# Optimization experiments

Hardware: AMD Instinct MI355X
Metric: run time of the kernel (lower is better)

## Reference

```python
import jax, jax.numpy as jnp
import numpy as np

N = 50000      # num nodes
E = 1600000    # num edges
F_IN = 512     # dataset.num_features
DIM = 512      # args.dim
C = 40         # dataset.num_classes


def setup_inputs() -> dict:
    key = jax.random.key(0)
    ks = jax.random.split(key, 5)
    x = jax.random.normal(ks[0], (N, F_IN), dtype=jnp.float32)
    edge_row = jax.random.randint(ks[1], (E,), 0, N, dtype=jnp.int64) if jax.config.jax_enable_x64 else jax.random.randint(ks[1], (E,), 0, N).astype(jnp.int32)
    edge_col = jax.random.randint(ks[2], (E,), 0, N).astype(edge_row.dtype)
    W1 = jax.random.normal(ks[3], (F_IN, DIM), dtype=jnp.float32) / np.float32(np.sqrt(F_IN))
    b1 = jnp.zeros((DIM,), jnp.float32)
    W2 = jax.random.normal(ks[4], (DIM * 5, C), dtype=jnp.float32) / np.float32(np.sqrt(DIM * 5))
    b2 = jnprz = jnp.zeros((C,), jnp.float32)
    return {"x": x, "edge_row": edge_row, "edge_col": edge_col,
            "W1": W1, "b1": b1, "W2": W2, "b2": b2}


def _gcn_norm(row, col, num_nodes):
    # PyG gcn_norm: add self-loops (weight 1), then D^-1/2 A D^-1/2
    loop = jnp.arange(num_nodes, dtype=row.dtype)
    row = jnp.concatenate([row, loop])
    col = jnp.concatenate([col, loop])
    ew = jnp.ones(row.shape[0], jnp.float32)
    deg = jax.ops.segment_sum(ew, col, num_segments=num_nodes)
    dinv = jnp.where(deg > 0, 1.0 / jnp.sqrt(deg), 0.0)
    val = dinv[row] * ew * dinv[col]
    return row, col, val


def _spmm(row, col, val, x):
    # out[i] = sum_{e: row[e]==i} val[e] * x[col[e]]
    return jax.ops.segment_sum(val[:, None] * x[col], row, num_segments=x.shape[0])


def reference(x, edge_row, edge_col, W1, b1, W2, b2):
    row, col, val = _gcn_norm(edge_row, edge_col, x.shape[0])
    t = jax.nn.relu(x @ W1 + b1)                      # [N, DIM]
    t1 = jnp.concatenate([t, _spmm(row, col, val, t)], axis=1)   # [N, 2*DIM]
    t2 = _spmm(row, col, val, t1)                     # [N, 2*DIM]
    h = jnp.concatenate([t, t1, t2], axis=1)          # [N, 5*DIM]
    # dropout treated as identity (deterministic eval reference)
    logits = h @ W2 + b2                              # [N, C]
    return jax.nn.log_softmax(logits, axis=1)
```

## Files before the change

kernel.cpp:

```cpp
#include <hip/hip_runtime.h>
#include <stdint.h>

#define NN 50000
#define NE 1600000
#define FI 512
#define DD 512
#define NC 40
#define SCAN_NB 49
#define CB 256
#define EPB (NE / CB)
#define HWRD 12500

typedef __attribute__((ext_vector_type(8))) short short8;
typedef __attribute__((ext_vector_type(4))) float float4v;
typedef __attribute__((ext_vector_type(2))) float f32x2;

static __device__ __forceinline__ unsigned short f2b(float f) {
    union { float f; unsigned int i; } v; v.f = f;
    unsigned int r = v.i + 0x7fffu + ((v.i >> 16) & 1u);
    return (unsigned short)(r >> 16);
}
static __device__ __forceinline__ float blo(unsigned int u) {
    union { unsigned int i; float f; } v; v.i = u << 16; return v.f;
}
static __device__ __forceinline__ float bhi(unsigned int u) {
    union { unsigned int i; float f; } v; v.i = u & 0xffff0000u; return v.f;
}
static __device__ __forceinline__ void async_copy16(void* lds, const void* g) {
    __builtin_amdgcn_global_load_lds((const __attribute__((address_space(1))) void*)g,
                                     (__attribute__((address_space(3))) void*)lds, 16, 0, 0);
}

__global__ __launch_bounds__(256) void mega1_kernel(
    const int* __restrict__ er, const int* __restrict__ ec,
    const float* __restrict__ x, const float* __restrict__ W1, const float* __restrict__ W2,
    unsigned char* __restrict__ rank, unsigned* __restrict__ hist_row, unsigned* __restrict__ hist_col,
    unsigned short* __restrict__ xb, unsigned short* __restrict__ w1t, unsigned short* __restrict__ wcpt) {
    __shared__ unsigned hb[HWRD];
    int bid = blockIdx.x, tid = threadIdx.x;
    if (bid < 2 * CB) {
        for (int w = tid; w < HWRD; w += 256) hb[w] = 0;
        __syncthreads();
        int b = bid & (CB - 1);
        int e0 = b * EPB;
        if (bid < CB) {
            for (int e = e0 + tid; e < e0 + EPB; e += 256) {
                int r = er[e];
                unsigned sh = (r & 3) * 8;
                unsigned old = atomicAdd(&hb[r >> 2], 1u << sh);
                rank[e] = (unsigned char)((old >> sh) & 0xFFu);
            }
        } else {
            for (int e = e0 + tid; e < e0 + EPB; e += 256) {
                int c = ec[e];
                atomicAdd(&hb[c >> 2], 1u << ((c & 3) * 8));
            }
        }
        __syncthreads();
        unsigned* dst = (bid < CB ? hist_row : hist_col) + (size_t)b * HWRD;
        for (int w = tid; w < HWRD; w += 256) dst[w] = hb[w];
        return;
    }
    bid -= 2 * CB;
    if (bid < 12500) {
        int t = bid * 256 + tid;
        const float* xf = x + (size_t)t * 8;
        float4 v0 = *(const float4*)(xf);
        float4 v1 = *(const float4*)(xf + 4);
        uint4 u;
        u.x = ((unsigned)f2b(v0.y) << 16) | f2b(v0.x);
        u.y = ((unsigned)f2b(v0.w) << 16) | f2b(v0.z);
        u.z = ((unsigned)f2b(v1.y) << 16) | f2b(v1.x);
        u.w = ((unsigned)f2b(v1.w) << 16) | f2b(v1.z);
        *(uint4*)(xb + (size_t)t * 8) = u;
        return;
    }
    bid -= 12500;
    if (bid < 1024) {
        int t = bid * 256 + tid;
        int n = t & 511, k = t >> 9;
        w1t[n * 512 + k] = f2b(W1[(size_t)k * 512 + n]);
        return;
    }
    bid -= 1024;
    {
        int t = bid * 256 + tid;
        int n = t >> 9, k = t & 511;
        float v = 0.f;
        if (n < 40)       v = W2[(size_t)k * NC + n] + W2[(size_t)(k + 512) * NC + n];
        else if (n < 80)  v = W2[(size_t)(k + 1024) * NC + (n - 40)] + W2[(size_t)(k + 1536) * NC + (n - 40)];
        else if (n < 120) v = W2[(size_t)(k + 2048) * NC + (n - 80)];
        wcpt[n * 512 + k] = f2b(v);
    }
}

__global__ __launch_bounds__(256) void prep_kernel(
    const unsigned* __restrict__ hist_row, const unsigned* __restrict__ hist_col,
    unsigned* __restrict__ base_words, int* __restrict__ cntI, int* __restrict__ degI) {
    int t = blockIdx.x * 256 + threadIdx.x;
    if (t < HWRD) {
        unsigned acc = 0;
        for (int b = 0; b < CB; ++b) {
            unsigned h = hist_row[(size_t)b * HWRD + t];
            base_words[(size_t)b * HWRD + t] = acc;
            acc += h;
        }
        int4 o; o.x = acc & 0xFF; o.y = (acc >> 8) & 0xFF; o.z = (acc >> 16) & 0xFF; o.w = (acc >> 24) & 0xFF;
        ((int4*)cntI)[t] = o;
    } else if (t < 2 * HWRD) {
        int w = t - HWRD;
        unsigned acc = 0;
        for (int b = 0; b < CB; ++b) acc += hist_col[(size_t)b * HWRD + w];
        int4 o; o.x = acc & 0xFF; o.y = (acc >> 8) & 0xFF; o.z = (acc >> 16) & 0xFF; o.w = (acc >> 24) & 0xFF;
        ((int4*)degI)[w] = o;
    }
}

__global__ __launch_bounds__(1024) void scan1_kernel(const int* __restrict__ cnt,
                                                     int* __restrict__ excl, int* __restrict__ bsum) {
    __shared__ int buf[1024];
    int tid = threadIdx.x, gid = blockIdx.x * 1024 + tid;
    int v = (gid < NN) ? cnt[gid] : 0;
    buf[tid] = v;
    __syncthreads();
    int acc = v;
    for (int off = 1; off < 1024; off <<= 1) {
        int t = (tid >= off) ? buf[tid - off] : 0;
        __syncthreads();
        acc += t;
        buf[tid] = acc;
        __syncthreads();
    }
    if (gid < NN) excl[gid] = acc - v;
    if (tid == 1023) bsum[blockIdx.x] = acc;
}

__global__ void scan2_kernel(const int* __restrict__ bsum, int* __restrict__ boff) {
    int tid = threadIdx.x;
    int orig = (tid < SCAN_NB) ? bsum[tid] : 0;
    int v = orig;
    #pragma unroll
    for (int off = 1; off < 64; off <<= 1) {
        int t = __shfl_up(v, off, 64);
        if (tid >= off) v += t;
    }
    if (tid < SCAN_NB) boff[tid] = v - orig;
}

__global__ void scan3_kernel(int* __restrict__ rowptr, const int* __restrict__ boff,
                             const int* __restrict__ deg, float* __restrict__ dinv) {
    int gid = blockIdx.x * 256 + threadIdx.x;
    if (gid < NN) {
        rowptr[gid] += boff[gid >> 10];
        dinv[gid] = rsqrtf((float)(deg[gid] + 1));
    }
    if (gid == 0) rowptr[NN] = NE;
}

__global__ __launch_bounds__(256) void mega2_kernel(
    const int* __restrict__ er, const int* __restrict__ ec, const int* __restrict__ rowptr,
    const unsigned char* __restrict__ rank, const unsigned char* __restrict__ base8,
    int* __restrict__ colss,
    const unsigned short* __restrict__ xb, const unsigned short* __restrict__ w1t,
    const float* __restrict__ b1, unsigned short* __restrict__ tbuf) {
    __shared__ __align__(16) unsigned short As[128 * 32];
    __shared__ __align__(16) unsigned short Bs[128 * 32];
    int bid = blockIdx.x;
    if (bid < CB) {
        int tid = threadIdx.x;
        const unsigned char* bb = base8 + (size_t)bid * 50000;
        int e0 = bid * EPB;
        int e = e0 + tid;
        #pragma unroll 4
        for (int it = 0; it < EPB / 256; ++it, e += 256) {
            int r = er[e], c = ec[e];
            colss[rowptr[r] + (int)bb[r] + (int)rank[e]] = c;
        }
        if (e < e0 + EPB) {
            int r = er[e], c = ec[e];
            colss[rowptr[r] + (int)bb[r] + (int)rank[e]] = c;
        }
        return;
    }
    bid -= CB;
    const int m0 = (bid >> 2) * 128, n0 = (bid & 3) * 128;
    const int tid = threadIdx.x;
    const int wave = tid >> 6, lane = tid & 63;
    const int q = lane >> 4, c = lane & 15;
    const int wm = wave & 1, wn = wave >> 1;

    float4v acc[4][4];
    for (int i = 0; i < 4; ++i)
        for (int j = 0; j < 4; ++j)
            acc[i][j] = (float4v){0.f, 0.f, 0.f, 0.f};

    for (int k0 = 0; k0 < FI; k0 += 32) {
        __syncthreads();
        #pragma unroll
        for (int h = 0; h < 2; ++h) {
            int chunk = h * 256 + wave * 64 + lane;
            int r = chunk >> 2, kc = chunk & 3;
            int gm = m0 + r; gm = gm < NN ? gm : NN - 1;
            async_copy16((char*)As + (size_t)(h * 256 + wave * 64) * 16,
                         xb + (size_t)gm * FI + k0 + kc * 8);
            async_copy16((char*)Bs + (size_t)(h * 256 + wave * 64) * 16,
                         w1t + (size_t)(n0 + r) * FI + k0 + kc * 8);
        }
        __syncthreads();
        short8 a[4], b[4];
        #pragma unroll
        for (int mi = 0; mi < 4; ++mi)
            a[mi] = *(const short8*)(As + ((wm * 64 + mi * 16 + c) * 32 + q * 8));
        #pragma unroll
        for (int ni = 0; ni < 4; ++ni)
            b[ni] = *(const short8*)(Bs + ((wn * 64 + ni * 16 + c) * 32 + q * 8));
        #pragma unroll
        for (int mi = 0; mi < 4; ++mi)
            #pragma unroll
            for (int ni = 0; ni < 4; ++ni)
                acc[mi][ni] = __builtin_amdgcn_mfma_f32_16x16x32_bf16(a[mi], b[ni], acc[mi][ni], 0, 0, 0);
    }
    #pragma unroll
    for (int ni = 0; ni < 4; ++ni) {
        int col = n0 + wn * 64 + ni * 16 + c;
        float bias = b1[col];
        #pragma unroll
        for (int mi = 0; mi < 4; ++mi) {
            int rbase = m0 + wm * 64 + mi * 16 + q * 4;
            #pragma unroll
            for (int r = 0; r < 4; ++r) {
                int row = rbase + r;
                if (row < NN) {
                    float v = acc[mi][ni][r] + bias;
                    v = v > 0.f ? v : 0.f;
                    tbuf[(size_t)row * FI + col] = f2b(v);
                }
            }
        }
    }
}

__global__ __launch_bounds__(256) void proj_kernel(
    const unsigned short* __restrict__ tb, const unsigned short* __restrict__ wcpt,
    const float* __restrict__ dinv, float* __restrict__ d0f,
    unsigned short* __restrict__ zs12p) {
    int wave = threadIdx.x >> 6, lane = threadIdx.x & 63;
    int q = lane >> 4, c = lane & 15;
    int row0 = blockIdx.x * 64 + wave * 16;
    int ra = row0 + c; ra = ra < NN ? ra : NN - 1;
    const unsigned short* ap = tb + (size_t)ra * FI + q * 8;

    float4v A[8];
    #pragma unroll
    for (int g = 0; g < 8; ++g) A[g] = (float4v){0.f, 0.f, 0.f, 0.f};
    #pragma unroll 2
    for (int k0 = 0; k0 < 512; k0 += 32) {
        short8 a = *(const short8*)(ap + k0);
        #pragma unroll
        for (int g = 0; g < 8; ++g) {
            short8 b = *(const short8*)(wcpt + (size_t)(g * 16 + c) * 512 + q * 8 + k0);
            A[g] = __builtin_amdgcn_mfma_f32_16x16x32_bf16(a, b, A[g], 0, 0, 0);
        }
    }
    #pragma unroll
    for (int r = 0; r < 4; ++r) {
        int rowg = row0 + q * 4 + r;
        if (rowg < NN) {
            float dv = dinv[rowg];
            #pragma unroll
            for (int g = 0; g < 8; ++g) {
                int j = g * 16 + c;
                float pv = A[g][r];
                if (j < 40)      d0f[(size_t)rowg * 40 + j] = pv;
                else if (j < 80) zs12p[(size_t)rowg * 128 + (j - 40)] = f2b(dv * pv);
                else             zs12p[(size_t)rowg * 128 + (j - 16)] = f2b(dv * pv);
            }
        }
    }
    for (int idx = lane; idx < 16 * 40; idx += 64) {
        int rr = row0 + idx / 40, pc = idx % 40;
        if (rr < NN) zs12p[(size_t)rr * 128 + (pc < 24 ? 40 + pc : 88 + pc)] = 0;
    }
}

__global__ __launch_bounds__(256) void spmma_kernel(
    const unsigned* __restrict__ zs,
    const int* __restrict__ rowptr, const int* __restrict__ cols,
    const float* __restrict__ dinv,
    float* __restrict__ u1b,
    unsigned* __restrict__ wpb) {
    int i = blockIdx.x * 4 + (threadIdx.x >> 6);
    if (i >= NN) return;
    int lane = threadIdx.x & 63;
    int h = lane >> 5, l = lane & 31;
    const float di = dinv[i];
    const unsigned* base = zs + l * 2;

    float a0 = 0.f, a1 = 0.f, a2 = 0.f, a3 = 0.f;
    float b0 = 0.f, b1 = 0.f, b2 = 0.f, b3 = 0.f;
    if (h == 0) {
        uint2 u = *(const uint2*)(zs + (size_t)i * 64 + l * 2);
        a0 = blo(u.x); a1 = bhi(u.x); a2 = blo(u.y); a3 = bhi(u.y);
    }
    int k = rowptr[i], e = rowptr[i + 1];
    for (; k + 8 <= e; k += 8) {
        int c0 = cols[k + h], c1 = cols[k + 2 + h], c2 = cols[k + 4 + h], c3 = cols[k + 6 + h];
        uint2 g0 = *(const uint2*)(base + (size_t)c0 * 64);
        uint2 g1 = *(const uint2*)(base + (size_t)c1 * 64);
        uint2 g2 = *(const uint2*)(base + (size_t)c2 * 64);
        uint2 g3 = *(const uint2*)(base + (size_t)c3 * 64);
        a0 += blo(g0.x); a1 += bhi(g0.x); a2 += blo(g0.y); a3 += bhi(g0.y);
        b0 += blo(g1.x); b1 += bhi(g1.x); b2 += blo(g1.y); b3 += bhi(g1.y);
        a0 += blo(g2.x); a1 += bhi(g2.x); a2 += blo(g2.y); a3 += bhi(g2.y);
        b0 += blo(g3.x); b1 += bhi(g3.x); b2 += blo(g3.y); b3 += bhi(g3.y);
    }
    for (; k + 2 <= e; k += 2) {
        int cc = cols[k + h];
        uint2 g = *(const uint2*)(base + (size_t)cc * 64);
        a0 += blo(g.x); a1 += bhi(g.x); a2 += blo(g.y); a3 += bhi(g.y);
    }
    if (k < e && h == 0) {
        int cc = cols[k];
        uint2 g = *(const uint2*)(base + (size_t)cc * 64);
        a0 += blo(g.x); a1 += bhi(g.x); a2 += blo(g.y); a3 += bhi(g.y);
    }
    a0 += b0; a1 += b1; a2 += b2; a3 += b3;
    a0 += __shfl_xor(a0, 32, 64); a1 += __shfl_xor(a1, 32, 64);
    a2 += __shfl_xor(a2, 32, 64); a3 += __shfl_xor(a3, 32, 64);
    if (h == 0) {
        if (l < 10) {
            float4 o; o.x = di * a0; o.y = di * a1; o.z = di * a2; o.w = di * a3;
            *(float4*)(u1b + (size_t)i * 40 + l * 4) = o;
        } else if (l >= 16) {
            float s = di * di;
            uint2 o;
            o.x = ((unsigned)f2b(s * a1) << 16) | f2b(s * a0);
            o.y = ((unsigned)f2b(s * a3) << 16) | f2b(s * a2);
            *(uint2*)(wpb + (size_t)i * 32 + (size_t)(l - 16) * 2) = o;
        }
    }
}

__global__ __launch_bounds__(256) void spmmb_kernel(
    const unsigned* __restrict__ wpb,
    const int* __restrict__ rowptr, const int* __restrict__ cols,
    const float* __restrict__ dinv, const float* __restrict__ d0f,
    const float* __restrict__ u1b, const float* __restrict__ b2p,
    float* __restrict__ out) {
    int i = blockIdx.x * 4 + (threadIdx.x >> 6);
    if (i >= NN) return;
    int lane = threadIdx.x & 63;
    int q = lane >> 4, l = lane & 15;
    const float di = dinv[i];
    const unsigned* base = wpb + l * 2;

    float a0 = 0.f, a1 = 0.f, a2 = 0.f, a3 = 0.f;
    float b0 = 0.f, b1 = 0.f, b2 = 0.f, b3 = 0.f;
    if (q == 0) {
        uint2 u = *(const uint2*)(wpb + (size_t)i * 32 + l * 2);
        a0 = blo(u.x); a1 = bhi(u.x); a2 = blo(u.y); a3 = bhi(u.y);
    }
    int k = rowptr[i], e = rowptr[i + 1];
    for (; k + 8 <= e; k += 8) {
        int c0 = cols[k + q], c1 = cols[k + 4 + q];
        uint2 g0 = *(const uint2*)(base + (size_t)c0 * 32);
        uint2 g1 = *(const uint2*)(base + (size_t)c1 * 32);
        a0 += blo(g0.x); a1 += bhi(g0.x); a2 += blo(g0.y); a3 += bhi(g0.y);
        b0 += blo(g1.x); b1 += bhi(g1.x); b2 += blo(g1.y); b3 += bhi(g1.y);
    }
    for (; k + 4 <= e; k += 4) {
        int cc = cols[k + q];
        uint2 g = *(const uint2*)(base + (size_t)cc * 32);
        a0 += blo(g.x); a1 += bhi(g.x); a2 += blo(g.y); a3 += bhi(g.y);
    }
    if (k + q < e) {
        int cc = cols[k + q];
        uint2 g = *(const uint2*)(base + (size_t)cc * 32);
        a0 += blo(g.x); a1 += bhi(g.x); a2 += blo(g.y); a3 += bhi(g.y);
    }
    a0 += b0; a1 += b1; a2 += b2; a3 += b3;
    a0 += __shfl_xor(a0, 16, 64); a1 += __shfl_xor(a1, 16, 64);
    a2 += __shfl_xor(a2, 16, 64); a3 += __shfl_xor(a3, 16, 64);
    a0 += __shfl_xor(a0, 32, 64); a1 += __shfl_xor(a1, 32, 64);
    a2 += __shfl_xor(a2, 32, 64); a3 += __shfl_xor(a3, 32, 64);

    float v0 = -1e30f, v1 = -1e30f, v2 = -1e30f, v3 = -1e30f;
    bool act = (q == 0) && (l < 10);
    if (act) {
        float4 dd = *(const float4*)(d0f + (size_t)i * 40 + l * 4);
        float4 uu = *(const float4*)(u1b + (size_t)i * 40 + l * 4);
        float4 bb = *(const float4*)(b2p + l * 4);
        v0 = dd.x + uu.x + di * a0 + bb.x;
        v1 = dd.y + uu.y + di * a1 + bb.y;
        v2 = dd.z + uu.z + di * a2 + bb.z;
        v3 = dd.w + uu.w + di * a3 + bb.w;
    }
    float mx = fmaxf(fmaxf(v0, v1), fmaxf(v2, v3));
    #pragma unroll
    for (int d = 1; d < 64; d <<= 1) mx = fmaxf(mx, __shfl_xor(mx, d, 64));
    float s = act ? (__expf(v0 - mx) + __expf(v1 - mx) + __expf(v2 - mx) + __expf(v3 - mx)) : 0.f;
    #pragma unroll
    for (int d = 1; d < 64; d <<= 1) s += __shfl_xor(s, d, 64);
    float lse = mx + __logf(s);
    if (act) {
        float4 o; o.x = v0 - lse; o.y = v1 - lse; o.z = v2 - lse; o.w = v3 - lse;
        *(float4*)(out + (size_t)i * 40 + l * 4) = o;
    }
}

extern "C" void kernel_launch(void* const* d_in, const int* in_sizes, int n_in,
                              void* d_out, int out_size, void* d_ws, size_t ws_size,
                              hipStream_t stream) {
    const float* x  = (const float*)d_in[0];
    const int*   er = (const int*)d_in[1];
    const int*   ec = (const int*)d_in[2];
    const float* W1 = (const float*)d_in[3];
    const float* b1 = (const float*)d_in[4];
    const float* W2 = (const float*)d_in[5];
    const float* b2 = (const float*)d_in[6];
    float* out = (float*)d_out;

    char* p = (char*)d_ws;
    auto alloc = [&](size_t bytes) { char* r = p; p += (bytes + 255) & ~((size_t)255); return r; };
    int*      cntI   = (int*)      alloc((size_t)NN * 4);
    int*      degI   = (int*)      alloc((size_t)NN * 4);
    int*      rowptr = (int*)      alloc((size_t)(NN + 1) * 4);
    float*    dinv   = (float*)    alloc((size_t)NN * 4);
    int*      bsum   = (int*)      alloc((size_t)SCAN_NB * 4);
    int*      boff   = (int*)      alloc((size_t)SCAN_NB * 4);
    unsigned char* rank = (unsigned char*)alloc((size_t)NE);
    int*      colss  = (int*)      alloc((size_t)NE * 4);
    unsigned* hist_row = (unsigned*)alloc((size_t)CB * HWRD * 4);
    unsigned* hist_col = (unsigned*)alloc((size_t)CB * HWRD * 4);
    unsigned* base_w   = (unsigned*)alloc((size_t)CB * HWRD * 4);
    unsigned short* w1t  = (unsigned short*)alloc((size_t)512 * 512 * 2);
    unsigned short* wcpt = (unsigned short*)alloc((size_t)128 * 512 * 2);
    unsigned short* xb   = (unsigned short*)alloc((size_t)NN * FI * 2);
    unsigned short* tbuf = (unsigned short*)alloc((size_t)NN * FI * 2);
    unsigned short* zs12p = (unsigned short*)alloc((size_t)NN * 128 * 2);
    float*    d0f  = (float*)alloc((size_t)NN * 40 * 4);
    float*    u1b  = (float*)alloc((size_t)NN * 40 * 4);
    unsigned* wpb  = (unsigned*)alloc((size_t)NN * 32 * 4);

    mega1_kernel<<<2 * CB + 12500 + 1024 + 256, 256, 0, stream>>>(
        er, ec, x, W1, W2, rank, hist_row, hist_col, xb, w1t, wcpt);
    prep_kernel<<<(2 * HWRD + 255) / 256, 256, 0, stream>>>(hist_row, hist_col, base_w, cntI, degI);
    scan1_kernel<<<SCAN_NB, 1024, 0, stream>>>(cntI, rowptr, bsum);
    scan2_kernel<<<1, 64, 0, stream>>>(bsum, boff);
    scan3_kernel<<<(NN + 255) / 256, 256, 0, stream>>>(rowptr, boff, degI, dinv);
    mega2_kernel<<<CB + ((NN + 127) / 128) * 4, 256, 0, stream>>>(
        er, ec, rowptr, rank, (const unsigned char*)base_w, colss, xb, w1t, b1, tbuf);
    proj_kernel<<<(NN + 63) / 64, 256, 0, stream>>>(tbuf, wcpt, dinv, d0f, zs12p);
    spmma_kernel<<<(NN + 3) / 4, 256, 0, stream>>>((const unsigned*)zs12p, rowptr, colss, dinv, u1b, wpb);
    spmmb_kernel<<<(NN + 3) / 4, 256, 0, stream>>>(wpb, rowptr, colss, dinv, d0f, u1b, b2, out);
}
```

Before: 476.5 us.

## Compact sparse gather buffers and remap GEMM tiles to 128x64 with XCD-aware ordering

Shrinks the padded bf16 intermediate rows from 128 to 80 columns and the second-hop buffer from 32 to 20 words, so each SpMM gather moves fewer bytes per edge. The second SpMM now gives each lane 2 classes and splits edges across two half-waves instead of four quarter-waves. The first GEMM switches to 128x64 tiles and a block-index remap that groups M tiles by XCD, aiming for better L2 reuse of rows of x. The 80-column row stride is not a multiple of 128 bytes, so gathers may become less aligned, and the smaller tiles mean more blocks with less reuse per block.

```diff
diff --git a/kernel.cpp b/kernel.cpp
--- a/kernel.cpp
+++ b/kernel.cpp
@@ -10,6 +10,8 @@
 #define CB 256
 #define EPB (NE / CB)
 #define HWRD 12500
+#define MT 391
+#define GEMMB 3136
 
 typedef __attribute__((ext_vector_type(8))) short short8;
 typedef __attribute__((ext_vector_type(4))) float float4v;
@@ -164,7 +166,7 @@
     const unsigned short* __restrict__ xb, const unsigned short* __restrict__ w1t,
     const float* __restrict__ b1, unsigned short* __restrict__ tbuf) {
     __shared__ __align__(16) unsigned short As[128 * 32];
-    __shared__ __align__(16) unsigned short Bs[128 * 32];
+    __shared__ __align__(16) unsigned short Bs[64 * 32];
     int bid = blockIdx.x;
     if (bid < CB) {
         int tid = threadIdx.x;
@@ -182,16 +184,21 @@
         }
         return;
     }
-    bid -= CB;
-    const int m0 = (bid >> 2) * 128, n0 = (bid & 3) * 128;
+    int gb = bid - CB;
+    int xcd = gb & 7, slot = gb >> 3;
+    int m = xcd + 8 * (slot >> 3), n = slot & 7;
+    if (m >= MT) return;
+    const int m0 = m * 128, n0 = n * 64;
     const int tid = threadIdx.x;
     const int wave = tid >> 6, lane = tid & 63;
     const int q = lane >> 4, c = lane & 15;
     const int wm = wave & 1, wn = wave >> 1;
 
-    float4v acc[4][4];
+    float4v acc[4][2];
+    #pragma unroll
     for (int i = 0; i < 4; ++i)
-        for (int j = 0; j < 4; ++j)
+        #pragma unroll
+        for (int j = 0; j < 2; ++j)
             acc[i][j] = (float4v){0.f, 0.f, 0.f, 0.f};
 
     for (int k0 = 0; k0 < FI; k0 += 32) {
@@ -201,28 +208,32 @@
             int chunk = h * 256 + wave * 64 + lane;
             int r = chunk >> 2, kc = chunk & 3;
             int gm = m0 + r; gm = gm < NN ? gm : NN - 1;
-            async_copy16((char*)As + (size_t)(h * 256 + wave * 64) * 16,
+            async_copy16((char*)As + (size_t)chunk * 16,
                          xb + (size_t)gm * FI + k0 + kc * 8);
-            async_copy16((char*)Bs + (size_t)(h * 256 + wave * 64) * 16,
-                         w1t + (size_t)(n0 + r) * FI + k0 + kc * 8);
-        }
-        __syncthreads();
-        short8 a[4], b[4];
+        }
+        {
+            int chunk = wave * 64 + lane;
+            int rb = chunk >> 2, kb = chunk & 3;
+            async_copy16((char*)Bs + (size_t)chunk * 16,
+                         w1t + (size_t)(n0 + rb) * FI + k0 + kb * 8);
+        }
+        __syncthreads();
+        short8 a[4], b[2];
         #pragma unroll
         for (int mi = 0; mi < 4; ++mi)
             a[mi] = *(const short8*)(As + ((wm * 64 + mi * 16 + c) * 32 + q * 8));
         #pragma unroll
-        for (int ni = 0; ni < 4; ++ni)
-            b[ni] = *(const short8*)(Bs + ((wn * 64 + ni * 16 + c) * 32 + q * 8));
+        for (int ni = 0; ni < 2; ++ni)
+            b[ni] = *(const short8*)(Bs + ((wn * 32 + ni * 16 + c) * 32 + q * 8));
         #pragma unroll
         for (int mi = 0; mi < 4; ++mi)
             #pragma unroll
-            for (int ni = 0; ni < 4; ++ni)
+            for (int ni = 0; ni < 2; ++ni)
                 acc[mi][ni] = __builtin_amdgcn_mfma_f32_16x16x32_bf16(a[mi], b[ni], acc[mi][ni], 0, 0, 0);
     }
     #pragma unroll
-    for (int ni = 0; ni < 4; ++ni) {
-        int col = n0 + wn * 64 + ni * 16 + c;
+    for (int ni = 0; ni < 2; ++ni) {
+        int col = n0 + wn * 32 + ni * 16 + c;
         float bias = b1[col];
         #pragma unroll
         for (int mi = 0; mi < 4; ++mi) {
@@ -243,7 +254,7 @@
 __global__ __launch_bounds__(256) void proj_kernel(
     const unsigned short* __restrict__ tb, const unsigned short* __restrict__ wcpt,
     const float* __restrict__ dinv, float* __restrict__ d0f,
-    unsigned short* __restrict__ zs12p) {
+    unsigned short* __restrict__ zsp) {
     int wave = threadIdx.x >> 6, lane = threadIdx.x & 63;
     int q = lane >> 4, c = lane & 15;
     int row0 = blockIdx.x * 64 + wave * 16;
@@ -271,15 +282,10 @@
             for (int g = 0; g < 8; ++g) {
                 int j = g * 16 + c;
                 float pv = A[g][r];
-                if (j < 40)      d0f[(size_t)rowg * 40 + j] = pv;
-                else if (j < 80) zs12p[(size_t)rowg * 128 + (j - 40)] = f2b(dv * pv);
-                else             zs12p[(size_t)rowg * 128 + (j - 16)] = f2b(dv * pv);
+                if (j < 40)       d0f[(size_t)rowg * 40 + j] = pv;
+                else if (j < 120) zsp[(size_t)rowg * 80 + (j - 40)] = f2b(dv * pv);
             }
         }
-    }
-    for (int idx = lane; idx < 16 * 40; idx += 64) {
-        int rr = row0 + idx / 40, pc = idx % 40;
-        if (rr < NN) zs12p[(size_t)rr * 128 + (pc < 24 ? 40 + pc : 88 + pc)] = 0;
     }
 }
 
@@ -293,22 +299,23 @@
     if (i >= NN) return;
     int lane = threadIdx.x & 63;
     int h = lane >> 5, l = lane & 31;
+    if (l >= 20) return;
     const float di = dinv[i];
     const unsigned* base = zs + l * 2;
 
     float a0 = 0.f, a1 = 0.f, a2 = 0.f, a3 = 0.f;
     float b0 = 0.f, b1 = 0.f, b2 = 0.f, b3 = 0.f;
     if (h == 0) {
-        uint2 u = *(const uint2*)(zs + (size_t)i * 64 + l * 2);
+        uint2 u = *(const uint2*)(zs + (size_t)i * 40 + l * 2);
         a0 = blo(u.x); a1 = bhi(u.x); a2 = blo(u.y); a3 = bhi(u.y);
     }
     int k = rowptr[i], e = rowptr[i + 1];
     for (; k + 8 <= e; k += 8) {
         int c0 = cols[k + h], c1 = cols[k + 2 + h], c2 = cols[k + 4 + h], c3 = cols[k + 6 + h];
-        uint2 g0 = *(const uint2*)(base + (size_t)c0 * 64);
-        uint2 g1 = *(const uint2*)(base + (size_t)c1 * 64);
-        uint2 g2 = *(const uint2*)(base + (size_t)c2 * 64);
-        uint2 g3 = *(const uint2*)(base + (size_t)c3 * 64);
+        uint2 g0 = *(const uint2*)(base + (size_t)c0 * 40);
+        uint2 g1 = *(const uint2*)(base + (size_t)c1 * 40);
+        uint2 g2 = *(const uint2*)(base + (size_t)c2 * 40);
+        uint2 g3 = *(const uint2*)(base + (size_t)c3 * 40);
         a0 += blo(g0.x); a1 += bhi(g0.x); a2 += blo(g0.y); a3 += bhi(g0.y);
         b0 += blo(g1.x); b1 += bhi(g1.x); b2 += blo(g1.y); b3 += bhi(g1.y);
         a0 += blo(g2.x); a1 += bhi(g2.x); a2 += blo(g2.y); a3 += bhi(g2.y);
@@ -316,12 +323,12 @@
     }
     for (; k + 2 <= e; k += 2) {
         int cc = cols[k + h];
-        uint2 g = *(const uint2*)(base + (size_t)cc * 64);
+        uint2 g = *(const uint2*)(base + (size_t)cc * 40);
         a0 += blo(g.x); a1 += bhi(g.x); a2 += blo(g.y); a3 += bhi(g.y);
     }
     if (k < e && h == 0) {
         int cc = cols[k];
-        uint2 g = *(const uint2*)(base + (size_t)cc * 64);
+        uint2 g = *(const uint2*)(base + (size_t)cc * 40);
         a0 += blo(g.x); a1 += bhi(g.x); a2 += blo(g.y); a3 += bhi(g.y);
     }
     a0 += b0; a1 += b1; a2 += b2; a3 += b3;
@@ -331,12 +338,12 @@
         if (l < 10) {
             float4 o; o.x = di * a0; o.y = di * a1; o.z = di * a2; o.w = di * a3;
             *(float4*)(u1b + (size_t)i * 40 + l * 4) = o;
-        } else if (l >= 16) {
+        } else {
             float s = di * di;
             uint2 o;
             o.x = ((unsigned)f2b(s * a1) << 16) | f2b(s * a0);
             o.y = ((unsigned)f2b(s * a3) << 16) | f2b(s * a2);
-            *(uint2*)(wpb + (size_t)i * 32 + (size_t)(l - 16) * 2) = o;
+            *(uint2*)(wpb + (size_t)i * 20 + (size_t)(l - 10) * 2) = o;
         }
     }
 }
@@ -350,61 +357,61 @@
     int i = blockIdx.x * 4 + (threadIdx.x >> 6);
     if (i >= NN) return;
     int lane = threadIdx.x & 63;
-    int q = lane >> 4, l = lane & 15;
+    int h = lane >> 5, l = lane & 31;
     const float di = dinv[i];
-    const unsigned* base = wpb + l * 2;
-
-    float a0 = 0.f, a1 = 0.f, a2 = 0.f, a3 = 0.f;
-    float b0 = 0.f, b1 = 0.f, b2 = 0.f, b3 = 0.f;
-    if (q == 0) {
-        uint2 u = *(const uint2*)(wpb + (size_t)i * 32 + l * 2);
-        a0 = blo(u.x); a1 = bhi(u.x); a2 = blo(u.y); a3 = bhi(u.y);
-    }
-    int k = rowptr[i], e = rowptr[i + 1];
-    for (; k + 8 <= e; k += 8) {
-        int c0 = cols[k + q], c1 = cols[k + 4 + q];
-        uint2 g0 = *(const uint2*)(base + (size_t)c0 * 32);
-        uint2 g1 = *(const uint2*)(base + (size_t)c1 * 32);
-        a0 += blo(g0.x); a1 += bhi(g0.x); a2 += blo(g0.y); a3 += bhi(g0.y);
-        b0 += blo(g1.x); b1 += bhi(g1.x); b2 += blo(g1.y); b3 += bhi(g1.y);
-    }
-    for (; k + 4 <= e; k += 4) {
-        int cc = cols[k + q];
-        uint2 g = *(const uint2*)(base + (size_t)cc * 32);
-        a0 += blo(g.x); a1 += bhi(g.x); a2 += blo(g.y); a3 += bhi(g.y);
-    }
-    if (k + q < e) {
-        int cc = cols[k + q];
-        uint2 g = *(const uint2*)(base + (size_t)cc * 32);
-        a0 += blo(g.x); a1 += bhi(g.x); a2 += blo(g.y); a3 += bhi(g.y);
-    }
-    a0 += b0; a1 += b1; a2 += b2; a3 += b3;
-    a0 += __shfl_xor(a0, 16, 64); a1 += __shfl_xor(a1, 16, 64);
-    a2 += __shfl_xor(a2, 16, 64); a3 += __shfl_xor(a3, 16, 64);
-    a0 += __shfl_xor(a0, 32, 64); a1 += __shfl_xor(a1, 32, 64);
-    a2 += __shfl_xor(a2, 32, 64); a3 += __shfl_xor(a3, 32, 64);
-
-    float v0 = -1e30f, v1 = -1e30f, v2 = -1e30f, v3 = -1e30f;
-    bool act = (q == 0) && (l < 10);
+    bool lact = (l < 20);
+    const unsigned* base = wpb + l;
+
+    float a0 = 0.f, a1 = 0.f;
+    float b0 = 0.f, b1 = 0.f;
+    if (lact && h == 0) {
+        unsigned u = wpb[(size_t)i * 20 + l];
+        a0 = blo(u); a1 = bhi(u);
+    }
+    if (lact) {
+        int k = rowptr[i], e = rowptr[i + 1];
+        for (; k + 8 <= e; k += 8) {
+            int c0 = cols[k + h], c1 = cols[k + 2 + h], c2 = cols[k + 4 + h], c3 = cols[k + 6 + h];
+            unsigned g0 = base[(size_t)c0 * 20];
+            unsigned g1 = base[(size_t)c1 * 20];
+            unsigned g2 = base[(size_t)c2 * 20];
+            unsigned g3 = base[(size_t)c3 * 20];
+            a0 += blo(g0); a1 += bhi(g0);
+            b0 += blo(g1); b1 += bhi(g1);
+            a0 += blo(g2); a1 += bhi(g2);
+            b0 += blo(g3); b1 += bhi(g3);
+        }
+        for (; k + 2 <= e; k += 2) {
+            unsigned g = base[(size_t)cols[k + h] * 20];
+            a0 += blo(g); a1 += bhi(g);
+        }
+        if (k < e && h == 0) {
+            unsigned g = base[(size_t)cols[k] * 20];
+            a0 += blo(g); a1 += bhi(g);
+        }
+        a0 += b0; a1 += b1;
+        a0 += __shfl_xor(a0, 32, 64);
+        a1 += __shfl_xor(a1, 32, 64);
+    }
+    float vx = -1e30f, vy = -1e30f;
+    bool act = lact && (h == 0);
     if (act) {
-        float4 dd = *(const float4*)(d0f + (size_t)i * 40 + l * 4);
-        float4 uu = *(const float4*)(u1b + (size_t)i * 40 + l * 4);
-        float4 bb = *(const float4*)(b2p + l * 4);
-        v0 = dd.x + uu.x + di * a0 + bb.x;
-        v1 = dd.y + uu.y + di * a1 + bb.y;
-        v2 = dd.z + uu.z + di * a2 + bb.z;
-        v3 = dd.w + uu.w + di * a3 + bb.w;
-    }
-    float mx = fmaxf(fmaxf(v0, v1), fmaxf(v2, v3));
-    #pragma unroll
-    for (int d = 1; d < 64; d <<= 1) mx = fmaxf(mx, __shfl_xor(mx, d, 64));
-    float s = act ? (__expf(v0 - mx) + __expf(v1 - mx) + __expf(v2 - mx) + __expf(v3 - mx)) : 0.f;
-    #pragma unroll
-    for (int d = 1; d < 64; d <<= 1) s += __shfl_xor(s, d, 64);
+        float2 dd = *(const float2*)(d0f + (size_t)i * 40 + l * 2);
+        float2 uu = *(const float2*)(u1b + (size_t)i * 40 + l * 2);
+        float2 bb = *(const float2*)(b2p + l * 2);
+        vx = dd.x + uu.x + di * a0 + bb.x;
+        vy = dd.y + uu.y + di * a1 + bb.y;
+    }
+    float mx = fmaxf(vx, vy);
+    #pragma unroll
+    for (int d = 1; d < 32; d <<= 1) mx = fmaxf(mx, __shfl_xor(mx, d, 64));
+    float s = act ? (__expf(vx - mx) + __expf(vy - mx)) : 0.f;
+    #pragma unroll
+    for (int d = 1; d < 32; d <<= 1) s += __shfl_xor(s, d, 64);
     float lse = mx + __logf(s);
     if (act) {
-        float4 o; o.x = v0 - lse; o.y = v1 - lse; o.z = v2 - lse; o.w = v3 - lse;
-        *(float4*)(out + (size_t)i * 40 + l * 4) = o;
+        float2 o; o.x = vx - lse; o.y = vy - lse;
+        *(float2*)(out + (size_t)i * 40 + l * 2) = o;
     }
 }
 
@@ -437,10 +444,10 @@
     unsigned short* wcpt = (unsigned short*)alloc((size_t)128 * 512 * 2);
     unsigned short* xb   = (unsigned short*)alloc((size_t)NN * FI * 2);
     unsigned short* tbuf = (unsigned short*)alloc((size_t)NN * FI * 2);
-    unsigned short* zs12p = (unsigned short*)alloc((size_t)NN * 128 * 2);
+    unsigned short* zsp  = (unsigned short*)alloc((size_t)NN * 80 * 2);
     float*    d0f  = (float*)alloc((size_t)NN * 40 * 4);
     float*    u1b  = (float*)alloc((size_t)NN * 40 * 4);
-    unsigned* wpb  = (unsigned*)alloc((size_t)NN * 32 * 4);
+    unsigned* wpb  = (unsigned*)alloc((size_t)NN * 20 * 4);
 
     mega1_kernel<<<2 * CB + 12500 + 1024 + 256, 256, 0, stream>>>(
         er, ec, x, W1, W2, rank, hist_row, hist_col, xb, w1t, wcpt);
@@ -448,9 +455,9 @@
     scan1_kernel<<<SCAN_NB, 1024, 0, stream>>>(cntI, rowptr, bsum);
     scan2_kernel<<<1, 64, 0, stream>>>(bsum, boff);
     scan3_kernel<<<(NN + 255) / 256, 256, 0, stream>>>(rowptr, boff, degI, dinv);
-    mega2_kernel<<<CB + ((NN + 127) / 128) * 4, 256, 0, stream>>>(
+    mega2_kernel<<<CB + GEMMB, 256, 0, stream>>>(
         er, ec, rowptr, rank, (const unsigned char*)base_w, colss, xb, w1t, b1, tbuf);
-    proj_kernel<<<(NN + 63) / 64, 256, 0, stream>>>(tbuf, wcpt, dinv, d0f, zs12p);
-    spmma_kernel<<<(NN + 3) / 4, 256, 0, stream>>>((const unsigned*)zs12p, rowptr, colss, dinv, u1b, wpb);
+    proj_kernel<<<(NN + 63) / 64, 256, 0, stream>>>(tbuf, wcpt, dinv, d0f, zsp);
+    spmma_kernel<<<(NN + 3) / 4, 256, 0, stream>>>((const unsigned*)zsp, rowptr, colss, dinv, u1b, wpb);
     spmmb_kernel<<<(NN + 3) / 4, 256, 0, stream>>>(wpb, rowptr, colss, dinv, d0f, u1b, b2, out);
 }
```

Result: faster. 455.9 us (-4.3%).
